# Kernel tuning notes

Measured on AMD Instinct MI355X. Metric: run time of the kernel, lower is better.

The kernel has to match this reference:

```python
import jax, jax.numpy as jnp
import numpy as np

N = 50000
E = 800000
EPS = 1e-12


def sage_conv(x, src, dst, W_l, b_l, W_r):
    # PyG SAGEConv (mean aggr): out = lin_l(mean_{j in N(i)} x_j) + lin_r(x_i)
    msg = x[src]                                             # [E, d] gather
    agg = jax.ops.segment_sum(msg, dst, num_segments=N)      # [N, d]
    cnt = jax.ops.segment_sum(jnp.ones((E,), x.dtype), dst, num_segments=N)
    mean = agg / jnp.maximum(cnt, 1.0)[:, None]              # isolated nodes -> 0
    return mean @ W_l + b_l + x @ W_r


def setup_inputs() -> dict:
    key = jax.random.key(0)
    ks = jax.random.split(key, 12)
    s = 0.05
    return {
        "x": jax.random.normal(ks[0], (N, 128), dtype=jnp.float32),
        "edge_index": jax.random.randint(ks[1], (2, E), 0, N, dtype=jnp.int64),
        # pre: Linear(128 -> 128)
        "pre_W": jax.random.normal(ks[2], (128, 128), dtype=jnp.float32) * s,
        "pre_b": jnp.zeros((128,), dtype=jnp.float32),
        # conv_first: SAGEConv(128 -> 256)
        "W1_l": jax.random.normal(ks[3], (128, 256), dtype=jnp.float32) * s,
        "b1": jnp.zeros((256,), dtype=jnp.float32),
        "W1_r": jax.random.normal(ks[4], (128, 256), dtype=jnp.float32) * s,
        # conv_hidden[0]: SAGEConv(256 -> 256)
        "W2_l": jax.random.normal(ks[5], (256, 256), dtype=jnp.float32) * s,
        "b2": jnp.zeros((256,), dtype=jnp.float32),
        "W2_r": jax.random.normal(ks[6], (256, 256), dtype=jnp.float32) * s,
        # conv_out: SAGEConv(256 -> 256)
        "W3_l": jax.random.normal(ks[7], (256, 256), dtype=jnp.float32) * s,
        "b3": jnp.zeros((256,), dtype=jnp.float32),
        "W3_r": jax.random.normal(ks[8], (256, 256), dtype=jnp.float32) * s,
    }


def reference(x, edge_index, pre_W, pre_b, W1_l, b1, W1_r, W2_l, b2, W2_r, W3_l, b3, W3_r):
    src, dst = edge_index[0], edge_index[1]
    h = x @ pre_W + pre_b                                   # feature_pre Linear
    h = jax.nn.relu(sage_conv(h, src, dst, W1_l, b1, W1_r))  # dropout = identity (eval)
    h = jax.nn.relu(sage_conv(h, src, dst, W2_l, b2, W2_r))
    h = sage_conv(h, src, dst, W3_l, b3, W3_r)
    norm = jnp.sqrt(jnp.sum(h * h, axis=-1, keepdims=True))
    return h / jnp.maximum(norm, EPS)                       # F.normalize(p=2, dim=-1)
```

## Files before the change

kernel.cpp:

```cpp
#include <hip/hip_runtime.h>
#include <cstddef>
#include <cstdint>


typedef __attribute__((ext_vector_type(8))) short short8;
typedef __attribute__((ext_vector_type(4))) float f32x4;

__device__ __forceinline__ unsigned rne_bf16(float f) {
    unsigned b = __float_as_uint(f);
    return (b + 0x7fffu + ((b >> 16) & 1u)) >> 16;
}
__device__ __forceinline__ float bf16_lo(unsigned u) { return __uint_as_float(u << 16); }
__device__ __forceinline__ float bf16_hi(unsigned u) { return __uint_as_float(u & 0xffff0000u); }

__device__ __forceinline__ void stage16(const void* g, unsigned short* ldsbase,
                                        int lane) {
#if __has_builtin(__builtin_amdgcn_global_load_lds)
    (void)lane;
    __builtin_amdgcn_global_load_lds(
        (const __attribute__((address_space(1))) unsigned int*)g,
        (__attribute__((address_space(3))) unsigned int*)ldsbase, 16, 0, 0);
#else
    *(uint4*)(ldsbase + (size_t)lane * 8) = *(const uint4*)g;
#endif
}


__global__ __launch_bounds__(256) void deg_kernel(const int* __restrict__ dst,
                                                  int* __restrict__ deg, int E) {
    int e = blockIdx.x * 256 + threadIdx.x;
    if (e < E) atomicAdd(&deg[dst[e]], 1);
}

__global__ __launch_bounds__(256) void bsum_kernel(const int* __restrict__ deg,
                                                   int* __restrict__ bsum, int n) {
    int i = blockIdx.x * 256 + threadIdx.x;
    int v = (i < n) ? deg[i] : 0;
#pragma unroll
    for (int s = 32; s > 0; s >>= 1) v += __shfl_down(v, s);
    __shared__ int ws[4];
    int lane = threadIdx.x & 63, w = threadIdx.x >> 6;
    if (lane == 0) ws[w] = v;
    __syncthreads();
    if (threadIdx.x == 0) bsum[blockIdx.x] = ws[0] + ws[1] + ws[2] + ws[3];
}

__global__ __launch_bounds__(256) void bscan_kernel(const int* __restrict__ bsum,
                                                    int* __restrict__ boff,
                                                    int* __restrict__ off,
                                                    int nb, int n, int E) {
    int t = threadIdx.x;
    int v = (t < nb) ? bsum[t] : 0;
    int incl = v;
#pragma unroll
    for (int s = 1; s < 64; s <<= 1) {
        int u = __shfl_up(incl, s);
        if ((t & 63) >= s) incl += u;
    }
    __shared__ int ws[4];
    int lane = t & 63, w = t >> 6;
    if (lane == 63) ws[w] = incl;
    __syncthreads();
    int woff = 0;
    for (int j = 0; j < w; ++j) woff += ws[j];
    if (t < nb) boff[t] = woff + incl - v;
    if (t == 0) off[n] = E;
}

__global__ __launch_bounds__(256) void scan_kernel(const int* __restrict__ deg,
                                                   const int* __restrict__ boff,
                                                   int* __restrict__ off,
                                                   float* __restrict__ inv, int n) {
    int i = blockIdx.x * 256 + threadIdx.x;
    int v = (i < n) ? deg[i] : 0;
    int incl = v;
#pragma unroll
    for (int s = 1; s < 64; s <<= 1) {
        int u = __shfl_up(incl, s);
        if ((threadIdx.x & 63) >= s) incl += u;
    }
    __shared__ int ws[4];
    int lane = threadIdx.x & 63, w = threadIdx.x >> 6;
    if (lane == 63) ws[w] = incl;
    __syncthreads();
    int woff = 0;
    for (int j = 0; j < w; ++j) woff += ws[j];
    if (i < n) {
        off[i] = boff[blockIdx.x] + woff + incl - v;
        inv[i] = 1.0f / fmaxf((float)v, 1.0f);
    }
}

__global__ __launch_bounds__(256) void fill_kernel(const int* __restrict__ src,
                                                   const int* __restrict__ dst,
                                                   const int* __restrict__ off,
                                                   int* __restrict__ deg,
                                                   int* __restrict__ ssrc, int E) {
    int e = blockIdx.x * 256 + threadIdx.x;
    if (e >= E) return;
    int d = dst[e];
    int pos = off[d] + atomicSub(&deg[d], 1) - 1;
    ssrc[pos] = src[e];
}


__global__ __launch_bounds__(256) void prep_all(
    const float* __restrict__ x, uint2* __restrict__ xb, int n4, int XB,
    const float* __restrict__ pre_W, const float* __restrict__ W1_l,
    const float* __restrict__ W1_r, const float* __restrict__ W2_l,
    const float* __restrict__ W2_r, const float* __restrict__ W3_l,
    const float* __restrict__ W3_r,
    unsigned short* __restrict__ WT0, unsigned short* __restrict__ WT1,
    unsigned short* __restrict__ WT2, unsigned short* __restrict__ WT3,
    unsigned short* __restrict__ WT4, unsigned short* __restrict__ WT5,
    unsigned short* __restrict__ WT6) {
    if (blockIdx.x < (unsigned)XB) {
        int i = blockIdx.x * 256 + threadIdx.x;
        if (i >= n4) return;
        float4 v = ((const float4*)x)[i];
        uint2 o;
        o.x = rne_bf16(v.x) | (rne_bf16(v.y) << 16);
        o.y = rne_bf16(v.z) | (rne_bf16(v.w) << 16);
        xb[i] = o;
        return;
    }
    int idx = (blockIdx.x - XB) * 256 + threadIdx.x;
    if (idx < 16384) {
        int k = idx >> 7, n = idx & 127;
        WT0[n * 128 + k] = (unsigned short)rne_bf16(pre_W[idx]);
        return;
    }
    idx -= 16384;
    if (idx < 32768) {
        int k = idx >> 8, n = idx & 255;
        WT1[n * 128 + k] = (unsigned short)rne_bf16(W1_l[idx]);
        return;
    }
    idx -= 32768;
    if (idx < 32768) {
        int k = idx >> 8, n = idx & 255;
        WT2[n * 128 + k] = (unsigned short)rne_bf16(W1_r[idx]);
        return;
    }
    idx -= 32768;
    if (idx < 65536) {
        int k = idx >> 8, n = idx & 255;
        WT3[n * 256 + k] = (unsigned short)rne_bf16(W2_l[idx]);
        return;
    }
    idx -= 65536;
    if (idx < 65536) {
        int k = idx >> 8, n = idx & 255;
        WT4[n * 256 + k] = (unsigned short)rne_bf16(W2_r[idx]);
        return;
    }
    idx -= 65536;
    if (idx < 65536) {
        int k = idx >> 8, n = idx & 255;
        WT5[n * 256 + k] = (unsigned short)rne_bf16(W3_l[idx]);
        return;
    }
    idx -= 65536;
    if (idx < 65536) {
        int k = idx >> 8, n = idx & 255;
        WT6[n * 256 + k] = (unsigned short)rne_bf16(W3_r[idx]);
    }
}


template <int D>
__global__ __launch_bounds__(256) void gather_b(const unsigned short* __restrict__ h,
                                                const int* __restrict__ off,
                                                const int* __restrict__ ssrc,
                                                const float* __restrict__ inv,
                                                unsigned short* __restrict__ agg, int n) {
    int node = blockIdx.x * 4 + (threadIdx.x >> 6);
    if (node >= n) return;
    int lane = threadIdx.x & 63;
    int beg = off[node], end = off[node + 1];
    float sc = inv[node];

    if (D == 256) {
        const int half = lane >> 5;
        const int sub  = lane & 31;
        const unsigned short* col = h + (sub << 3);
        float a[8] = {0, 0, 0, 0, 0, 0, 0, 0};
        float b[8] = {0, 0, 0, 0, 0, 0, 0, 0};
        int k = beg;
        for (; k + 3 < end; k += 4) {
            int s0 = ssrc[k + half];
            int s1 = ssrc[k + 2 + half];
            uint4 u = *(const uint4*)(col + (size_t)s0 * 256);
            uint4 v = *(const uint4*)(col + (size_t)s1 * 256);
            a[0] += bf16_lo(u.x); a[1] += bf16_hi(u.x);
            a[2] += bf16_lo(u.y); a[3] += bf16_hi(u.y);
            a[4] += bf16_lo(u.z); a[5] += bf16_hi(u.z);
            a[6] += bf16_lo(u.w); a[7] += bf16_hi(u.w);
            b[0] += bf16_lo(v.x); b[1] += bf16_hi(v.x);
            b[2] += bf16_lo(v.y); b[3] += bf16_hi(v.y);
            b[4] += bf16_lo(v.z); b[5] += bf16_hi(v.z);
            b[6] += bf16_lo(v.w); b[7] += bf16_hi(v.w);
        }
        for (; k < end; k += 2) {
            int e = k + half;
            if (e < end) {
                uint4 u = *(const uint4*)(col + (size_t)ssrc[e] * 256);
                a[0] += bf16_lo(u.x); a[1] += bf16_hi(u.x);
                a[2] += bf16_lo(u.y); a[3] += bf16_hi(u.y);
                a[4] += bf16_lo(u.z); a[5] += bf16_hi(u.z);
                a[6] += bf16_lo(u.w); a[7] += bf16_hi(u.w);
            }
        }
#pragma unroll
        for (int i = 0; i < 8; ++i) a[i] += b[i];
#pragma unroll
        for (int i = 0; i < 8; ++i) a[i] += __shfl_xor(a[i], 32);
        if (half == 0) {
#pragma unroll
            for (int i = 0; i < 8; ++i) a[i] *= sc;
            uint4 o;
            o.x = rne_bf16(a[0]) | (rne_bf16(a[1]) << 16);
            o.y = rne_bf16(a[2]) | (rne_bf16(a[3]) << 16);
            o.z = rne_bf16(a[4]) | (rne_bf16(a[5]) << 16);
            o.w = rne_bf16(a[6]) | (rne_bf16(a[7]) << 16);
            *(uint4*)(agg + (size_t)node * 256 + (sub << 3)) = o;
        }
    } else {
        const int q   = lane >> 4;
        const int sub = lane & 15;
        const unsigned short* col = h + (sub << 3);
        float a[8] = {0, 0, 0, 0, 0, 0, 0, 0};
        float b[8] = {0, 0, 0, 0, 0, 0, 0, 0};
        int k = beg;
        for (; k + 7 < end; k += 8) {
            int s0 = ssrc[k + q];
            int s1 = ssrc[k + 4 + q];
            uint4 u = *(const uint4*)(col + (size_t)s0 * 128);
            uint4 v = *(const uint4*)(col + (size_t)s1 * 128);
            a[0] += bf16_lo(u.x); a[1] += bf16_hi(u.x);
            a[2] += bf16_lo(u.y); a[3] += bf16_hi(u.y);
            a[4] += bf16_lo(u.z); a[5] += bf16_hi(u.z);
            a[6] += bf16_lo(u.w); a[7] += bf16_hi(u.w);
            b[0] += bf16_lo(v.x); b[1] += bf16_hi(v.x);
            b[2] += bf16_lo(v.y); b[3] += bf16_hi(v.y);
            b[4] += bf16_lo(v.z); b[5] += bf16_hi(v.z);
            b[6] += bf16_lo(v.w); b[7] += bf16_hi(v.w);
        }
        for (; k < end; k += 4) {
            int e = k + q;
            if (e < end) {
                uint4 u = *(const uint4*)(col + (size_t)ssrc[e] * 128);
                a[0] += bf16_lo(u.x); a[1] += bf16_hi(u.x);
                a[2] += bf16_lo(u.y); a[3] += bf16_hi(u.y);
                a[4] += bf16_lo(u.z); a[5] += bf16_hi(u.z);
                a[6] += bf16_lo(u.w); a[7] += bf16_hi(u.w);
            }
        }
#pragma unroll
        for (int i = 0; i < 8; ++i) a[i] += b[i];
#pragma unroll
        for (int i = 0; i < 8; ++i) a[i] += __shfl_xor(a[i], 16);
#pragma unroll
        for (int i = 0; i < 8; ++i) a[i] += __shfl_xor(a[i], 32);
        if (q == 0) {
#pragma unroll
            for (int i = 0; i < 8; ++i) a[i] *= sc;
            uint4 o;
            o.x = rne_bf16(a[0]) | (rne_bf16(a[1]) << 16);
            o.y = rne_bf16(a[2]) | (rne_bf16(a[3]) << 16);
            o.z = rne_bf16(a[4]) | (rne_bf16(a[5]) << 16);
            o.w = rne_bf16(a[6]) | (rne_bf16(a[7]) << 16);
            *(uint4*)(agg + (size_t)node * 128 + (sub << 3)) = o;
        }
    }
}

__global__ __launch_bounds__(256) void gemm_bt(
    const unsigned short* __restrict__ A1, const unsigned short* __restrict__ W1T,
    const float* __restrict__ bias, unsigned short* __restrict__ outb,
    int M, int K, int Nn) {
    __shared__ __align__(16) unsigned short As[128 * 64];
    __shared__ __align__(16) unsigned short Bs[128 * 64];

    const int t = threadIdx.x;
    const int lane = t & 63;
    const int w = t >> 6;
    const int wm = w >> 1, wn = w & 1;
    const int m0 = blockIdx.x * 128;
    const int n0 = blockIdx.y * 128;

    f32x4 acc[4][4];
#pragma unroll
    for (int i = 0; i < 4; ++i)
#pragma unroll
        for (int j = 0; j < 4; ++j) acc[i][j] = (f32x4){0.f, 0.f, 0.f, 0.f};

    for (int k0 = 0; k0 < K; k0 += 64) {
#pragma unroll
        for (int r = 0; r < 4; ++r) {
            int p = r * 256 + t;
            int row = p >> 3, slot = p & 7;
            int c = slot ^ (row & 7);
            int gm = m0 + row;
            if (gm >= M) gm = M - 1;
            uint4 va = *(const uint4*)(A1 + (size_t)gm * K + k0 + c * 8);
            uint4 vb = *(const uint4*)(W1T + (size_t)(n0 + row) * K + k0 + c * 8);
            *(uint4*)&As[(size_t)p * 8] = va;
            *(uint4*)&Bs[(size_t)p * 8] = vb;
        }
        __syncthreads();
#pragma unroll
        for (int kk = 0; kk < 2; ++kk) {
            short8 af[4], bfr[4];
            int ac = kk * 4 + (lane >> 4);
#pragma unroll
            for (int i = 0; i < 4; ++i) {
                int arow = wm * 64 + i * 16 + (lane & 15);
                af[i] = *(const short8*)&As[arow * 64 + ((ac ^ (arow & 7)) << 3)];
                int brow = wn * 64 + i * 16 + (lane & 15);
                bfr[i] = *(const short8*)&Bs[brow * 64 + ((ac ^ (brow & 7)) << 3)];
            }
#pragma unroll
            for (int mi = 0; mi < 4; ++mi)
#pragma unroll
                for (int ni = 0; ni < 4; ++ni)
                    acc[mi][ni] = __builtin_amdgcn_mfma_f32_16x16x32_bf16(
                        af[mi], bfr[ni], acc[mi][ni], 0, 0, 0);
        }
        __syncthreads();
    }

#pragma unroll
    for (int ni = 0; ni < 4; ++ni) {
        int n = n0 + wn * 64 + ni * 16 + (lane & 15);
        float bv = (bias != nullptr) ? bias[n] : 0.0f;
#pragma unroll
        for (int mi = 0; mi < 4; ++mi) {
            int mbase = m0 + wm * 64 + mi * 16 + ((lane >> 4) << 2);
#pragma unroll
            for (int r = 0; r < 4; ++r) {
                int m = mbase + r;
                if (m >= M) continue;
                outb[(size_t)m * Nn + n] = (unsigned short)rne_bf16(acc[mi][ni][r] + bv);
            }
        }
    }
}

__global__ __launch_bounds__(512) void gemm_wide(
    const unsigned short* __restrict__ A1, const unsigned short* __restrict__ W1T,
    const unsigned short* __restrict__ A2, const unsigned short* __restrict__ W2T,
    const float* __restrict__ bias,
    unsigned short* __restrict__ outb, float* __restrict__ outf,
    int M, int K, int relu) {
    __shared__ __align__(16) unsigned short As[128 * 64];
    __shared__ __align__(16) unsigned short Bs[256 * 64];
    __shared__ float rs[128][4];

    const int t = threadIdx.x;
    const int lane = t & 63;
    const int w8 = t >> 6;
    const int wm = w8 >> 2, wn = w8 & 3;
    const int m0 = blockIdx.x * 128;

    f32x4 acc[4][4];
#pragma unroll
    for (int i = 0; i < 4; ++i)
#pragma unroll
        for (int j = 0; j < 4; ++j) acc[i][j] = (f32x4){0.f, 0.f, 0.f, 0.f};

    for (int pass = 0; pass < 2; ++pass) {
        const unsigned short* A = pass ? A2 : A1;
        const unsigned short* W = pass ? W2T : W1T;

        for (int k0 = 0; k0 < K; k0 += 64) {
#pragma unroll
            for (int i = 0; i < 2; ++i) {
                int base = (w8 * 2 + i) * 64;
                int p = base + lane;
                int row = p >> 3, slot = p & 7;
                int c = slot ^ (row & 7);
                int gm = m0 + row;
                if (gm >= M) gm = M - 1;
                stage16(A + (size_t)gm * K + k0 + c * 8, &As[(size_t)base * 8], lane);
            }
#pragma unroll
            for (int i = 0; i < 4; ++i) {
                int base = (w8 * 4 + i) * 64;
                int p = base + lane;
                int row = p >> 3, slot = p & 7;
                int c = slot ^ (row & 7);
                stage16(W + (size_t)row * K + k0 + c * 8, &Bs[(size_t)base * 8], lane);
            }
            __syncthreads();
#pragma unroll
            for (int kk = 0; kk < 2; ++kk) {
                short8 af[4], bfr[4];
                int ac = kk * 4 + (lane >> 4);
#pragma unroll
                for (int i = 0; i < 4; ++i) {
                    int arow = wm * 64 + i * 16 + (lane & 15);
                    af[i] = *(const short8*)&As[arow * 64 + ((ac ^ (arow & 7)) << 3)];
                    int brow = wn * 64 + i * 16 + (lane & 15);
                    bfr[i] = *(const short8*)&Bs[brow * 64 + ((ac ^ (brow & 7)) << 3)];
                }
#pragma unroll
                for (int mi = 0; mi < 4; ++mi)
#pragma unroll
                    for (int ni = 0; ni < 4; ++ni)
                        acc[mi][ni] = __builtin_amdgcn_mfma_f32_16x16x32_bf16(
                            af[mi], bfr[ni], acc[mi][ni], 0, 0, 0);
            }
            __syncthreads();
        }
    }

    if (outb) {
#pragma unroll
        for (int ni = 0; ni < 4; ++ni) {
            int n = wn * 64 + ni * 16 + (lane & 15);
            float bv = bias[n];
#pragma unroll
            for (int mi = 0; mi < 4; ++mi) {
                int mbase = m0 + wm * 64 + mi * 16 + ((lane >> 4) << 2);
#pragma unroll
                for (int r = 0; r < 4; ++r) {
                    int m = mbase + r;
                    if (m >= M) continue;
                    float v = acc[mi][ni][r] + bv;
                    if (relu) v = fmaxf(v, 0.0f);
                    outb[(size_t)m * 256 + n] = (unsigned short)rne_bf16(v);
                }
            }
        }
        return;
    }

#pragma unroll
    for (int ni = 0; ni < 4; ++ni) {
        float bv = bias[wn * 64 + ni * 16 + (lane & 15)];
#pragma unroll
        for (int mi = 0; mi < 4; ++mi)
#pragma unroll
            for (int r = 0; r < 4; ++r) acc[mi][ni][r] += bv;
    }
#pragma unroll
    for (int mi = 0; mi < 4; ++mi) {
#pragma unroll
        for (int r = 0; r < 4; ++r) {
            float p = acc[mi][0][r] * acc[mi][0][r] + acc[mi][1][r] * acc[mi][1][r] +
                      acc[mi][2][r] * acc[mi][2][r] + acc[mi][3][r] * acc[mi][3][r];
            p += __shfl_xor(p, 1);
            p += __shfl_xor(p, 2);
            p += __shfl_xor(p, 4);
            p += __shfl_xor(p, 8);
            if ((lane & 15) == 0)
                rs[wm * 64 + mi * 16 + ((lane >> 4) << 2) + r][wn] = p;
        }
    }
    __syncthreads();
#pragma unroll
    for (int mi = 0; mi < 4; ++mi) {
        int mbase = m0 + wm * 64 + mi * 16 + ((lane >> 4) << 2);
        int lrow = wm * 64 + mi * 16 + ((lane >> 4) << 2);
#pragma unroll
        for (int r = 0; r < 4; ++r) {
            int m = mbase + r;
            if (m >= M) continue;
            float s = rs[lrow + r][0] + rs[lrow + r][1] + rs[lrow + r][2] + rs[lrow + r][3];
            float sc = 1.0f / fmaxf(sqrtf(s), 1e-12f);
#pragma unroll
            for (int ni = 0; ni < 4; ++ni) {
                int n = wn * 64 + ni * 16 + (lane & 15);
                outf[(size_t)m * 256 + n] = acc[mi][ni][r] * sc;
            }
        }
    }
}

extern "C" void kernel_launch(void* const* d_in, const int* in_sizes, int n_in,
                              void* d_out, int out_size, void* d_ws, size_t ws_size,
                              hipStream_t stream) {
    const int N = 50000;
    const int E = 800000;
    const int NB = (N + 255) / 256;

    const float* x     = (const float*)d_in[0];
    const int*   ei    = (const int*)d_in[1];
    const float* pre_W = (const float*)d_in[2];
    const float* pre_b = (const float*)d_in[3];
    const float* W1_l  = (const float*)d_in[4];
    const float* b1    = (const float*)d_in[5];
    const float* W1_r  = (const float*)d_in[6];
    const float* W2_l  = (const float*)d_in[7];
    const float* b2    = (const float*)d_in[8];
    const float* W2_r  = (const float*)d_in[9];
    const float* W3_l  = (const float*)d_in[10];
    const float* b3    = (const float*)d_in[11];
    const float* W3_r  = (const float*)d_in[12];
    float* out = (float*)d_out;

    const int* src = ei;
    const int* dst = ei + E;

    int* deg  = (int*)d_ws;
    int* off  = deg + N;
    int* bsum = off + N + 1;
    int* boff = bsum + 256;
    int* ssrc = boff + 256;
    size_t int_words = (size_t)2 * N + 1 + 512 + E;
    int_words = (int_words + 3) & ~(size_t)3;

    float* inv = (float*)d_ws + int_words;
    unsigned short* us = (unsigned short*)(inv + N);

    unsigned short* xb  = us;                 us += (size_t)N * 128;
    unsigned short* WT0 = us;                 us += 16384;
    unsigned short* WT1 = us;                 us += 32768;
    unsigned short* WT2 = us;                 us += 32768;
    unsigned short* WT3 = us;                 us += 65536;
    unsigned short* WT4 = us;                 us += 65536;
    unsigned short* WT5 = us;                 us += 65536;
    unsigned short* WT6 = us;                 us += 65536;
    unsigned short* h0b   = us;               us += (size_t)N * 128;
    unsigned short* agg1b = us;               us += (size_t)N * 128;
    unsigned short* h1b   = us;               us += (size_t)N * 256;
    unsigned short* agg2b = us;               us += (size_t)N * 256;
    unsigned short* h2b   = us;               us += (size_t)N * 256;
    unsigned short* agg3b = us;               us += (size_t)N * 256;

    hipMemsetAsync(deg, 0, (size_t)N * sizeof(int), stream);
    deg_kernel<<<(E + 255) / 256, 256, 0, stream>>>(dst, deg, E);
    bsum_kernel<<<NB, 256, 0, stream>>>(deg, bsum, N);
    bscan_kernel<<<1, 256, 0, stream>>>(bsum, boff, off, NB, N, E);
    scan_kernel<<<NB, 256, 0, stream>>>(deg, boff, off, inv, N);
    fill_kernel<<<(E + 255) / 256, 256, 0, stream>>>(src, dst, off, deg, ssrc, E);

    const int n4 = N * 128 / 4;
    const int XB = (n4 + 255) / 256;
    const int WB = (344064 + 255) / 256;
    prep_all<<<XB + WB, 256, 0, stream>>>(x, (uint2*)xb, n4, XB,
                                          pre_W, W1_l, W1_r, W2_l, W2_r, W3_l,
                                          W3_r, WT0, WT1, WT2, WT3, WT4, WT5, WT6);

    const int MT = (N + 127) / 128;
    const int AG = (N + 3) / 4;

    gemm_bt<<<dim3(MT, 1), 256, 0, stream>>>(xb, WT0, pre_b, h0b, N, 128, 128);

    gather_b<128><<<AG, 256, 0, stream>>>(h0b, off, ssrc, inv, agg1b, N);
    gemm_wide<<<MT, 512, 0, stream>>>(agg1b, WT1, h0b, WT2, b1, h1b, nullptr,
                                      N, 128, 1);

    gather_b<256><<<AG, 256, 0, stream>>>(h1b, off, ssrc, inv, agg2b, N);
    gemm_wide<<<MT, 512, 0, stream>>>(agg2b, WT3, h1b, WT4, b2, h2b, nullptr,
                                      N, 256, 1);

    gather_b<256><<<AG, 256, 0, stream>>>(h2b, off, ssrc, inv, agg3b, N);
    gemm_wide<<<MT, 512, 0, stream>>>(agg3b, WT5, h2b, WT6, b3, nullptr, out,
                                      N, 256, 0);
}
```

Baseline: 497.1 us.

## Co-schedule independent GEMM and gather/CSR work in fused launches

The degree-count kernel is merged into the prep kernel, and the CSR fill kernel into the pre-linear GEMM, as extra block ranges of a single launch. In each SAGE layer the root-weight GEMM (x @ W_r + b) now runs in the same launch as the neighbour gather, with its result written to an fp32 scratch buffer. The follow-up GEMM does only the aggregated-neighbour half and adds that scratch. The aim is to overlap independent memory-bound and compute-bound work and to cut launch count. The cost is an extra fp32 N×256 buffer that is written and read back each layer.

```diff
diff --git a/kernel.cpp b/kernel.cpp
--- a/kernel.cpp
+++ b/kernel.cpp
@@ -26,12 +26,6 @@
 }
 
 
-__global__ __launch_bounds__(256) void deg_kernel(const int* __restrict__ dst,
-                                                  int* __restrict__ deg, int E) {
-    int e = blockIdx.x * 256 + threadIdx.x;
-    if (e < E) atomicAdd(&deg[dst[e]], 1);
-}
-
 __global__ __launch_bounds__(256) void bsum_kernel(const int* __restrict__ deg,
                                                    int* __restrict__ bsum, int n) {
     int i = blockIdx.x * 256 + threadIdx.x;
@@ -91,21 +85,9 @@
     }
 }
 
-__global__ __launch_bounds__(256) void fill_kernel(const int* __restrict__ src,
-                                                   const int* __restrict__ dst,
-                                                   const int* __restrict__ off,
-                                                   int* __restrict__ deg,
-                                                   int* __restrict__ ssrc, int E) {
-    int e = blockIdx.x * 256 + threadIdx.x;
-    if (e >= E) return;
-    int d = dst[e];
-    int pos = off[d] + atomicSub(&deg[d], 1) - 1;
-    ssrc[pos] = src[e];
-}
-
-
-__global__ __launch_bounds__(256) void prep_all(
-    const float* __restrict__ x, uint2* __restrict__ xb, int n4, int XB,
+
+__global__ __launch_bounds__(256) void fatA(
+    const float* __restrict__ x, uint2* __restrict__ xb, int n4, int XB, int PB,
     const float* __restrict__ pre_W, const float* __restrict__ W1_l,
     const float* __restrict__ W1_r, const float* __restrict__ W2_l,
     const float* __restrict__ W2_r, const float* __restrict__ W3_l,
@@ -113,7 +95,13 @@
     unsigned short* __restrict__ WT0, unsigned short* __restrict__ WT1,
     unsigned short* __restrict__ WT2, unsigned short* __restrict__ WT3,
     unsigned short* __restrict__ WT4, unsigned short* __restrict__ WT5,
-    unsigned short* __restrict__ WT6) {
+    unsigned short* __restrict__ WT6,
+    const int* __restrict__ dst, int* __restrict__ deg, int E) {
+    if (blockIdx.x >= (unsigned)PB) {
+        int e = (blockIdx.x - PB) * 256 + threadIdx.x;
+        if (e < E) atomicAdd(&deg[dst[e]], 1);
+        return;
+    }
     if (blockIdx.x < (unsigned)XB) {
         int i = blockIdx.x * 256 + threadIdx.x;
         if (i >= n4) return;
@@ -167,14 +155,114 @@
     }
 }
 
+__device__ __forceinline__ void gemm128_body(
+    unsigned short* As, unsigned short* Bs,
+    const unsigned short* __restrict__ A, const unsigned short* __restrict__ WT,
+    const float* __restrict__ bias, float* __restrict__ Yout,
+    unsigned short* __restrict__ outb, int M, int K, int Nn, int m0, int n0) {
+    const int t = threadIdx.x;
+    const int lane = t & 63;
+    const int w = t >> 6;
+    const int wm = w >> 1, wn = w & 1;
+
+    f32x4 acc[4][4];
+#pragma unroll
+    for (int i = 0; i < 4; ++i)
+#pragma unroll
+        for (int j = 0; j < 4; ++j) acc[i][j] = (f32x4){0.f, 0.f, 0.f, 0.f};
+
+    for (int k0 = 0; k0 < K; k0 += 64) {
+#pragma unroll
+        for (int r = 0; r < 4; ++r) {
+            int p = r * 256 + t;
+            int row = p >> 3, slot = p & 7;
+            int c = slot ^ (row & 7);
+            int gm = m0 + row;
+            if (gm >= M) gm = M - 1;
+            uint4 va = *(const uint4*)(A + (size_t)gm * K + k0 + c * 8);
+            uint4 vb = *(const uint4*)(WT + (size_t)(n0 + row) * K + k0 + c * 8);
+            *(uint4*)&As[(size_t)p * 8] = va;
+            *(uint4*)&Bs[(size_t)p * 8] = vb;
+        }
+        __syncthreads();
+#pragma unroll
+        for (int kk = 0; kk < 2; ++kk) {
+            short8 af[4], bfr[4];
+            int ac = kk * 4 + (lane >> 4);
+#pragma unroll
+            for (int i = 0; i < 4; ++i) {
+                int arow = wm * 64 + i * 16 + (lane & 15);
+                af[i] = *(const short8*)&As[arow * 64 + ((ac ^ (arow & 7)) << 3)];
+                int brow = wn * 64 + i * 16 + (lane & 15);
+                bfr[i] = *(const short8*)&Bs[brow * 64 + ((ac ^ (brow & 7)) << 3)];
+            }
+#pragma unroll
+            for (int mi = 0; mi < 4; ++mi)
+#pragma unroll
+                for (int ni = 0; ni < 4; ++ni)
+                    acc[mi][ni] = __builtin_amdgcn_mfma_f32_16x16x32_bf16(
+                        af[mi], bfr[ni], acc[mi][ni], 0, 0, 0);
+        }
+        __syncthreads();
+    }
+
+#pragma unroll
+    for (int ni = 0; ni < 4; ++ni) {
+        int n = n0 + wn * 64 + ni * 16 + (lane & 15);
+        float bv = bias[n];
+#pragma unroll
+        for (int mi = 0; mi < 4; ++mi) {
+            int mbase = m0 + wm * 64 + mi * 16 + ((lane >> 4) << 2);
+#pragma unroll
+            for (int r = 0; r < 4; ++r) {
+                int m = mbase + r;
+                if (m >= M) continue;
+                float v = acc[mi][ni][r] + bv;
+                if (Yout) Yout[(size_t)m * Nn + n] = v;
+                else      outb[(size_t)m * Nn + n] = (unsigned short)rne_bf16(v);
+            }
+        }
+    }
+}
+
+
+__global__ __launch_bounds__(256) void fatB(
+    const unsigned short* __restrict__ xb, const unsigned short* __restrict__ WT0,
+    const float* __restrict__ pre_b, unsigned short* __restrict__ h0b, int M,
+    int GB,
+    const int* __restrict__ src, const int* __restrict__ dst,
+    const int* __restrict__ off, int* __restrict__ deg,
+    int* __restrict__ ssrc, int E) {
+    __shared__ __align__(16) unsigned short As[128 * 64];
+    __shared__ __align__(16) unsigned short Bs[128 * 64];
+    if (blockIdx.x < (unsigned)GB) {
+        gemm128_body(As, Bs, xb, WT0, pre_b, nullptr, h0b, M, 128, 128,
+                     blockIdx.x * 128, 0);
+        return;
+    }
+    int e = (blockIdx.x - GB) * 256 + threadIdx.x;
+    if (e >= E) return;
+    int d = dst[e];
+    int pos = off[d] + atomicSub(&deg[d], 1) - 1;
+    ssrc[pos] = src[e];
+}
+
 
 template <int D>
-__global__ __launch_bounds__(256) void gather_b(const unsigned short* __restrict__ h,
-                                                const int* __restrict__ off,
-                                                const int* __restrict__ ssrc,
-                                                const float* __restrict__ inv,
-                                                unsigned short* __restrict__ agg, int n) {
-    int node = blockIdx.x * 4 + (threadIdx.x >> 6);
+__global__ __launch_bounds__(256) void fat_gy(
+    const unsigned short* __restrict__ h, const unsigned short* __restrict__ WrT,
+    const float* __restrict__ bias, float* __restrict__ Yf, int M, int K, int GB,
+    const int* __restrict__ off, const int* __restrict__ ssrc,
+    const float* __restrict__ inv, unsigned short* __restrict__ agg, int n) {
+    __shared__ __align__(16) unsigned short As[128 * 64];
+    __shared__ __align__(16) unsigned short Bs[128 * 64];
+    if (blockIdx.x < (unsigned)GB) {
+        int p = blockIdx.x;
+        gemm128_body(As, Bs, h, WrT, bias, Yf, nullptr, M, K, 256,
+                     (p >> 1) * 128, (p & 1) * 128);
+        return;
+    }
+    int node = (blockIdx.x - GB) * 4 + (threadIdx.x >> 6);
     if (node >= n) return;
     int lane = threadIdx.x & 63;
     int beg = off[node], end = off[node + 1];
@@ -275,19 +363,20 @@
     }
 }
 
-__global__ __launch_bounds__(256) void gemm_bt(
-    const unsigned short* __restrict__ A1, const unsigned short* __restrict__ W1T,
-    const float* __restrict__ bias, unsigned short* __restrict__ outb,
-    int M, int K, int Nn) {
+__global__ __launch_bounds__(512) void gemm_lw(
+    const unsigned short* __restrict__ A, const unsigned short* __restrict__ WlT,
+    const float* __restrict__ Yf,
+    unsigned short* __restrict__ outb, float* __restrict__ outf,
+    int M, int K, int relu) {
     __shared__ __align__(16) unsigned short As[128 * 64];
-    __shared__ __align__(16) unsigned short Bs[128 * 64];
+    __shared__ __align__(16) unsigned short Bs[256 * 64];
+    __shared__ float rs[128][4];
 
     const int t = threadIdx.x;
     const int lane = t & 63;
-    const int w = t >> 6;
-    const int wm = w >> 1, wn = w & 1;
+    const int w8 = t >> 6;
+    const int wm = w8 >> 2, wn = w8 & 3;
     const int m0 = blockIdx.x * 128;
-    const int n0 = blockIdx.y * 128;
 
     f32x4 acc[4][4];
 #pragma unroll
@@ -297,16 +386,22 @@
 
     for (int k0 = 0; k0 < K; k0 += 64) {
 #pragma unroll
-        for (int r = 0; r < 4; ++r) {
-            int p = r * 256 + t;
+        for (int i = 0; i < 2; ++i) {
+            int base = (w8 * 2 + i) * 64;
+            int p = base + lane;
             int row = p >> 3, slot = p & 7;
             int c = slot ^ (row & 7);
             int gm = m0 + row;
             if (gm >= M) gm = M - 1;
-            uint4 va = *(const uint4*)(A1 + (size_t)gm * K + k0 + c * 8);
-            uint4 vb = *(const uint4*)(W1T + (size_t)(n0 + row) * K + k0 + c * 8);
-            *(uint4*)&As[(size_t)p * 8] = va;
-            *(uint4*)&Bs[(size_t)p * 8] = vb;
+            stage16(A + (size_t)gm * K + k0 + c * 8, &As[(size_t)base * 8], lane);
+        }
+#pragma unroll
+        for (int i = 0; i < 4; ++i) {
+            int base = (w8 * 4 + i) * 64;
+            int p = base + lane;
+            int row = p >> 3, slot = p & 7;
+            int c = slot ^ (row & 7);
+            stage16(WlT + (size_t)row * K + k0 + c * 8, &Bs[(size_t)base * 8], lane);
         }
         __syncthreads();
 #pragma unroll
@@ -332,86 +427,15 @@
 
 #pragma unroll
     for (int ni = 0; ni < 4; ++ni) {
-        int n = n0 + wn * 64 + ni * 16 + (lane & 15);
-        float bv = (bias != nullptr) ? bias[n] : 0.0f;
+        int n = wn * 64 + ni * 16 + (lane & 15);
 #pragma unroll
         for (int mi = 0; mi < 4; ++mi) {
             int mbase = m0 + wm * 64 + mi * 16 + ((lane >> 4) << 2);
 #pragma unroll
             for (int r = 0; r < 4; ++r) {
                 int m = mbase + r;
-                if (m >= M) continue;
-                outb[(size_t)m * Nn + n] = (unsigned short)rne_bf16(acc[mi][ni][r] + bv);
-            }
-        }
-    }
-}
-
-__global__ __launch_bounds__(512) void gemm_wide(
-    const unsigned short* __restrict__ A1, const unsigned short* __restrict__ W1T,
-    const unsigned short* __restrict__ A2, const unsigned short* __restrict__ W2T,
-    const float* __restrict__ bias,
-    unsigned short* __restrict__ outb, float* __restrict__ outf,
-    int M, int K, int relu) {
-    __shared__ __align__(16) unsigned short As[128 * 64];
-    __shared__ __align__(16) unsigned short Bs[256 * 64];
-    __shared__ float rs[128][4];
-
-    const int t = threadIdx.x;
-    const int lane = t & 63;
-    const int w8 = t >> 6;
-    const int wm = w8 >> 2, wn = w8 & 3;
-    const int m0 = blockIdx.x * 128;
-
-    f32x4 acc[4][4];
-#pragma unroll
-    for (int i = 0; i < 4; ++i)
-#pragma unroll
-        for (int j = 0; j < 4; ++j) acc[i][j] = (f32x4){0.f, 0.f, 0.f, 0.f};
-
-    for (int pass = 0; pass < 2; ++pass) {
-        const unsigned short* A = pass ? A2 : A1;
-        const unsigned short* W = pass ? W2T : W1T;
-
-        for (int k0 = 0; k0 < K; k0 += 64) {
-#pragma unroll
-            for (int i = 0; i < 2; ++i) {
-                int base = (w8 * 2 + i) * 64;
-                int p = base + lane;
-                int row = p >> 3, slot = p & 7;
-                int c = slot ^ (row & 7);
-                int gm = m0 + row;
-                if (gm >= M) gm = M - 1;
-                stage16(A + (size_t)gm * K + k0 + c * 8, &As[(size_t)base * 8], lane);
-            }
-#pragma unroll
-            for (int i = 0; i < 4; ++i) {
-                int base = (w8 * 4 + i) * 64;
-                int p = base + lane;
-                int row = p >> 3, slot = p & 7;
-                int c = slot ^ (row & 7);
-                stage16(W + (size_t)row * K + k0 + c * 8, &Bs[(size_t)base * 8], lane);
-            }
-            __syncthreads();
-#pragma unroll
-            for (int kk = 0; kk < 2; ++kk) {
-                short8 af[4], bfr[4];
-                int ac = kk * 4 + (lane >> 4);
-#pragma unroll
-                for (int i = 0; i < 4; ++i) {
-                    int arow = wm * 64 + i * 16 + (lane & 15);
-                    af[i] = *(const short8*)&As[arow * 64 + ((ac ^ (arow & 7)) << 3)];
-                    int brow = wn * 64 + i * 16 + (lane & 15);
-                    bfr[i] = *(const short8*)&Bs[brow * 64 + ((ac ^ (brow & 7)) << 3)];
-                }
-#pragma unroll
-                for (int mi = 0; mi < 4; ++mi)
-#pragma unroll
-                    for (int ni = 0; ni < 4; ++ni)
-                        acc[mi][ni] = __builtin_amdgcn_mfma_f32_16x16x32_bf16(
-                            af[mi], bfr[ni], acc[mi][ni], 0, 0, 0);
-            }
-            __syncthreads();
+                if (m < M) acc[mi][ni][r] += Yf[(size_t)m * 256 + n];
+            }
         }
     }
 
@@ -419,7 +443,6 @@
 #pragma unroll
         for (int ni = 0; ni < 4; ++ni) {
             int n = wn * 64 + ni * 16 + (lane & 15);
-            float bv = bias[n];
 #pragma unroll
             for (int mi = 0; mi < 4; ++mi) {
                 int mbase = m0 + wm * 64 + mi * 16 + ((lane >> 4) << 2);
@@ -427,7 +450,7 @@
                 for (int r = 0; r < 4; ++r) {
                     int m = mbase + r;
                     if (m >= M) continue;
-                    float v = acc[mi][ni][r] + bv;
+                    float v = acc[mi][ni][r];
                     if (relu) v = fmaxf(v, 0.0f);
                     outb[(size_t)m * 256 + n] = (unsigned short)rne_bf16(v);
                 }
@@ -436,14 +459,6 @@
         return;
     }
 
-#pragma unroll
-    for (int ni = 0; ni < 4; ++ni) {
-        float bv = bias[wn * 64 + ni * 16 + (lane & 15)];
-#pragma unroll
-        for (int mi = 0; mi < 4; ++mi)
-#pragma unroll
-            for (int r = 0; r < 4; ++r) acc[mi][ni][r] += bv;
-    }
 #pragma unroll
     for (int mi = 0; mi < 4; ++mi) {
 #pragma unroll
@@ -512,7 +527,8 @@
     int_words = (int_words + 3) & ~(size_t)3;
 
     float* inv = (float*)d_ws + int_words;
-    unsigned short* us = (unsigned short*)(inv + N);
+    float* Yf  = inv + N;
+    unsigned short* us = (unsigned short*)(Yf + (size_t)N * 256);
 
     unsigned short* xb  = us;                 us += (size_t)N * 128;
     unsigned short* WT0 = us;                 us += 16384;
@@ -529,34 +545,36 @@
     unsigned short* h2b   = us;               us += (size_t)N * 256;
     unsigned short* agg3b = us;               us += (size_t)N * 256;
 
+    const int MT = (N + 127) / 128;
+    const int AG = (N + 3) / 4;
+    const int GB = MT * 2;
+    const int n4 = N * 128 / 4;
+    const int XB = (n4 + 255) / 256;
+    const int WB = (344064 + 255) / 256;
+    const int PB = XB + WB;
+    const int DB = (E + 255) / 256;
+
     hipMemsetAsync(deg, 0, (size_t)N * sizeof(int), stream);
-    deg_kernel<<<(E + 255) / 256, 256, 0, stream>>>(dst, deg, E);
+    fatA<<<PB + DB, 256, 0, stream>>>(x, (uint2*)xb, n4, XB, PB,
+                                      pre_W, W1_l, W1_r, W2_l, W2_r, W3_l, W3_r,
+                                      WT0, WT1, WT2, WT3, WT4, WT5, WT6,
+                                      dst, deg, E);
     bsum_kernel<<<NB, 256, 0, stream>>>(deg, bsum, N);
     bscan_kernel<<<1, 256, 0, stream>>>(bsum, boff, off, NB, N, E);
     scan_kernel<<<NB, 256, 0, stream>>>(deg, boff, off, inv, N);
-    fill_kernel<<<(E + 255) / 256, 256, 0, stream>>>(src, dst, off, deg, ssrc, E);
-
-    const int n4 = N * 128 / 4;
-    const int XB = (n4 + 255) / 256;
-    const int WB = (344064 + 255) / 256;
-    prep_all<<<XB + WB, 256, 0, stream>>>(x, (uint2*)xb, n4, XB,
-                                          pre_W, W1_l, W1_r, W2_l, W2_r, W3_l,
-                                          W3_r, WT0, WT1, WT2, WT3, WT4, WT5, WT6);
-
-    const int MT = (N + 127) / 128;
-    const int AG = (N + 3) / 4;
-
-    gemm_bt<<<dim3(MT, 1), 256, 0, stream>>>(xb, WT0, pre_b, h0b, N, 128, 128);
-
-    gather_b<128><<<AG, 256, 0, stream>>>(h0b, off, ssrc, inv, agg1b, N);
-    gemm_wide<<<MT, 512, 0, stream>>>(agg1b, WT1, h0b, WT2, b1, h1b, nullptr,
-                                      N, 128, 1);
-
-    gather_b<256><<<AG, 256, 0, stream>>>(h1b, off, ssrc, inv, agg2b, N);
-    gemm_wide<<<MT, 512, 0, stream>>>(agg2b, WT3, h1b, WT4, b2, h2b, nullptr,
-                                      N, 256, 1);
-
-    gather_b<256><<<AG, 256, 0, stream>>>(h2b, off, ssrc, inv, agg3b, N);
-    gemm_wide<<<MT, 512, 0, stream>>>(agg3b, WT5, h2b, WT6, b3, nullptr, out,
-                                      N, 256, 0);
-}
+
+    fatB<<<MT + DB, 256, 0, stream>>>(xb, WT0, pre_b, h0b, N, MT,
+                                      src, dst, off, deg, ssrc, E);
+
+    fat_gy<128><<<GB + AG, 256, 0, stream>>>(h0b, WT2, b1, Yf, N, 128, GB,
+                                             off, ssrc, inv, agg1b, N);
+    gemm_lw<<<MT, 512, 0, stream>>>(agg1b, WT1, Yf, h1b, nullptr, N, 128, 1);
+
+    fat_gy<256><<<GB + AG, 256, 0, stream>>>(h1b, WT4, b2, Yf, N, 256, GB,
+                                             off, ssrc, inv, agg2b, N);
+    gemm_lw<<<MT, 512, 0, stream>>>(agg2b, WT3, Yf, h2b, nullptr, N, 256, 1);
+
+    fat_gy<256><<<GB + AG, 256, 0, stream>>>(h2b, WT6, b3, Yf, N, 256, GB,
+                                             off, ssrc, inv, agg3b, N);
+    gemm_lw<<<MT, 512, 0, stream>>>(agg3b, WT5, Yf, nullptr, out, N, 256, 0);
+}
```

Measured after the change: 633.4 us. 1.27x slower.

## Co-schedule root-weight GEMM with neighbor gather in one fused launch

Applied to the files above, without the earlier changes.

Each SAGE layer's x@W_r + bias term is now computed by extra blocks inside the gather kernel, so the independent MFMA work runs alongside the memory-bound neighbor aggregation. The result is written to an fp32 scratch buffer. The following GEMM does only the aggregated-mean @ W_l pass and adds that buffer in its epilogue. This halves the K-loop work of the post-gather GEMM and overlaps it with the gather. In exchange it adds an fp32 N×256 write and read per layer, and the new GEMM blocks load straight from global memory without LDS tiling.

```diff
diff --git a/kernel.cpp b/kernel.cpp
--- a/kernel.cpp
+++ b/kernel.cpp
@@ -167,16 +167,145 @@
     }
 }
 
+__global__ __launch_bounds__(256) void gemm_bt(
+    const unsigned short* __restrict__ A1, const unsigned short* __restrict__ W1T,
+    const float* __restrict__ bias, unsigned short* __restrict__ outb,
+    int M, int K, int Nn) {
+    __shared__ __align__(16) unsigned short As[128 * 64];
+    __shared__ __align__(16) unsigned short Bs[128 * 64];
+
+    const int t = threadIdx.x;
+    const int lane = t & 63;
+    const int w = t >> 6;
+    const int wm = w >> 1, wn = w & 1;
+    const int m0 = blockIdx.x * 128;
+    const int n0 = blockIdx.y * 128;
+
+    f32x4 acc[4][4];
+#pragma unroll
+    for (int i = 0; i < 4; ++i)
+#pragma unroll
+        for (int j = 0; j < 4; ++j) acc[i][j] = (f32x4){0.f, 0.f, 0.f, 0.f};
+
+    for (int k0 = 0; k0 < K; k0 += 64) {
+#pragma unroll
+        for (int r = 0; r < 4; ++r) {
+            int p = r * 256 + t;
+            int row = p >> 3, slot = p & 7;
+            int c = slot ^ (row & 7);
+            int gm = m0 + row;
+            if (gm >= M) gm = M - 1;
+            uint4 va = *(const uint4*)(A1 + (size_t)gm * K + k0 + c * 8);
+            uint4 vb = *(const uint4*)(W1T + (size_t)(n0 + row) * K + k0 + c * 8);
+            *(uint4*)&As[(size_t)p * 8] = va;
+            *(uint4*)&Bs[(size_t)p * 8] = vb;
+        }
+        __syncthreads();
+#pragma unroll
+        for (int kk = 0; kk < 2; ++kk) {
+            short8 af[4], bfr[4];
+            int ac = kk * 4 + (lane >> 4);
+#pragma unroll
+            for (int i = 0; i < 4; ++i) {
+                int arow = wm * 64 + i * 16 + (lane & 15);
+                af[i] = *(const short8*)&As[arow * 64 + ((ac ^ (arow & 7)) << 3)];
+                int brow = wn * 64 + i * 16 + (lane & 15);
+                bfr[i] = *(const short8*)&Bs[brow * 64 + ((ac ^ (brow & 7)) << 3)];
+            }
+#pragma unroll
+            for (int mi = 0; mi < 4; ++mi)
+#pragma unroll
+                for (int ni = 0; ni < 4; ++ni)
+                    acc[mi][ni] = __builtin_amdgcn_mfma_f32_16x16x32_bf16(
+                        af[mi], bfr[ni], acc[mi][ni], 0, 0, 0);
+        }
+        __syncthreads();
+    }
+
+#pragma unroll
+    for (int ni = 0; ni < 4; ++ni) {
+        int n = n0 + wn * 64 + ni * 16 + (lane & 15);
+        float bv = (bias != nullptr) ? bias[n] : 0.0f;
+#pragma unroll
+        for (int mi = 0; mi < 4; ++mi) {
+            int mbase = m0 + wm * 64 + mi * 16 + ((lane >> 4) << 2);
+#pragma unroll
+            for (int r = 0; r < 4; ++r) {
+                int m = mbase + r;
+                if (m >= M) continue;
+                outb[(size_t)m * Nn + n] = (unsigned short)rne_bf16(acc[mi][ni][r] + bv);
+            }
+        }
+    }
+}
+
 
 template <int D>
-__global__ __launch_bounds__(256) void gather_b(const unsigned short* __restrict__ h,
-                                                const int* __restrict__ off,
-                                                const int* __restrict__ ssrc,
-                                                const float* __restrict__ inv,
-                                                unsigned short* __restrict__ agg, int n) {
-    int node = blockIdx.x * 4 + (threadIdx.x >> 6);
+__global__ __launch_bounds__(256) void fat_gy(
+    const unsigned short* __restrict__ h, const unsigned short* __restrict__ WrT,
+    const float* __restrict__ bias, float* __restrict__ Yf, int M, int YB,
+    const int* __restrict__ off, const int* __restrict__ ssrc,
+    const float* __restrict__ inv, unsigned short* __restrict__ agg, int n) {
+    const int lane = threadIdx.x & 63;
+    if ((int)blockIdx.x < YB) {
+        const int p = blockIdx.x;
+        const int m0 = (p >> 1) * 64;
+        const int n0 = (p & 1) * 128;
+        const int w = threadIdx.x >> 6;
+        const int wm = w >> 1, wn = w & 1;
+        const int r16 = lane & 15, kq = lane >> 4;
+
+        f32x4 acc[2][4];
+#pragma unroll
+        for (int i = 0; i < 2; ++i)
+#pragma unroll
+            for (int j = 0; j < 4; ++j) acc[i][j] = (f32x4){0.f, 0.f, 0.f, 0.f};
+
+        int gm0 = m0 + wm * 32 + r16;
+        int gm1 = gm0 + 16;
+        if (gm0 >= M) gm0 = M - 1;
+        if (gm1 >= M) gm1 = M - 1;
+        const unsigned short* a0 = h + (size_t)gm0 * D + kq * 8;
+        const unsigned short* a1 = h + (size_t)gm1 * D + kq * 8;
+        const unsigned short* b0 = WrT + (size_t)(n0 + wn * 64 + r16) * D + kq * 8;
+
+#pragma unroll
+        for (int kk = 0; kk < D / 32; ++kk) {
+            short8 af0 = *(const short8*)(a0 + kk * 32);
+            short8 af1 = *(const short8*)(a1 + kk * 32);
+            short8 bf0 = *(const short8*)(b0 + kk * 32);
+            short8 bf1 = *(const short8*)(b0 + (size_t)16 * D + kk * 32);
+            short8 bf2 = *(const short8*)(b0 + (size_t)32 * D + kk * 32);
+            short8 bf3 = *(const short8*)(b0 + (size_t)48 * D + kk * 32);
+            acc[0][0] = __builtin_amdgcn_mfma_f32_16x16x32_bf16(af0, bf0, acc[0][0], 0, 0, 0);
+            acc[0][1] = __builtin_amdgcn_mfma_f32_16x16x32_bf16(af0, bf1, acc[0][1], 0, 0, 0);
+            acc[0][2] = __builtin_amdgcn_mfma_f32_16x16x32_bf16(af0, bf2, acc[0][2], 0, 0, 0);
+            acc[0][3] = __builtin_amdgcn_mfma_f32_16x16x32_bf16(af0, bf3, acc[0][3], 0, 0, 0);
+            acc[1][0] = __builtin_amdgcn_mfma_f32_16x16x32_bf16(af1, bf0, acc[1][0], 0, 0, 0);
+            acc[1][1] = __builtin_amdgcn_mfma_f32_16x16x32_bf16(af1, bf1, acc[1][1], 0, 0, 0);
+            acc[1][2] = __builtin_amdgcn_mfma_f32_16x16x32_bf16(af1, bf2, acc[1][2], 0, 0, 0);
+            acc[1][3] = __builtin_amdgcn_mfma_f32_16x16x32_bf16(af1, bf3, acc[1][3], 0, 0, 0);
+        }
+
+#pragma unroll
+        for (int j = 0; j < 4; ++j) {
+            int nn = n0 + wn * 64 + j * 16 + (lane & 15);
+            float bv = bias[nn];
+#pragma unroll
+            for (int i = 0; i < 2; ++i) {
+                int mbase = m0 + wm * 32 + i * 16 + ((lane >> 4) << 2);
+#pragma unroll
+                for (int r = 0; r < 4; ++r) {
+                    int m = mbase + r;
+                    if (m < M) Yf[(size_t)m * 256 + nn] = acc[i][j][r] + bv;
+                }
+            }
+        }
+        return;
+    }
+
+    int node = (blockIdx.x - YB) * 4 + (threadIdx.x >> 6);
     if (node >= n) return;
-    int lane = threadIdx.x & 63;
     int beg = off[node], end = off[node + 1];
     float sc = inv[node];
 
@@ -275,19 +404,20 @@
     }
 }
 
-__global__ __launch_bounds__(256) void gemm_bt(
-    const unsigned short* __restrict__ A1, const unsigned short* __restrict__ W1T,
-    const float* __restrict__ bias, unsigned short* __restrict__ outb,
-    int M, int K, int Nn) {
+__global__ __launch_bounds__(512) void gemm_lw(
+    const unsigned short* __restrict__ A, const unsigned short* __restrict__ WlT,
+    const float* __restrict__ Yf,
+    unsigned short* __restrict__ outb, float* __restrict__ outf,
+    int M, int K, int relu) {
     __shared__ __align__(16) unsigned short As[128 * 64];
-    __shared__ __align__(16) unsigned short Bs[128 * 64];
+    __shared__ __align__(16) unsigned short Bs[256 * 64];
+    __shared__ float rs[128][4];
 
     const int t = threadIdx.x;
     const int lane = t & 63;
-    const int w = t >> 6;
-    const int wm = w >> 1, wn = w & 1;
+    const int w8 = t >> 6;
+    const int wm = w8 >> 2, wn = w8 & 3;
     const int m0 = blockIdx.x * 128;
-    const int n0 = blockIdx.y * 128;
 
     f32x4 acc[4][4];
 #pragma unroll
@@ -297,16 +427,22 @@
 
     for (int k0 = 0; k0 < K; k0 += 64) {
 #pragma unroll
-        for (int r = 0; r < 4; ++r) {
-            int p = r * 256 + t;
+        for (int i = 0; i < 2; ++i) {
+            int base = (w8 * 2 + i) * 64;
+            int p = base + lane;
             int row = p >> 3, slot = p & 7;
             int c = slot ^ (row & 7);
             int gm = m0 + row;
             if (gm >= M) gm = M - 1;
-            uint4 va = *(const uint4*)(A1 + (size_t)gm * K + k0 + c * 8);
-            uint4 vb = *(const uint4*)(W1T + (size_t)(n0 + row) * K + k0 + c * 8);
-            *(uint4*)&As[(size_t)p * 8] = va;
-            *(uint4*)&Bs[(size_t)p * 8] = vb;
+            stage16(A + (size_t)gm * K + k0 + c * 8, &As[(size_t)base * 8], lane);
+        }
+#pragma unroll
+        for (int i = 0; i < 4; ++i) {
+            int base = (w8 * 4 + i) * 64;
+            int p = base + lane;
+            int row = p >> 3, slot = p & 7;
+            int c = slot ^ (row & 7);
+            stage16(WlT + (size_t)row * K + k0 + c * 8, &Bs[(size_t)base * 8], lane);
         }
         __syncthreads();
 #pragma unroll
@@ -332,86 +468,15 @@
 
 #pragma unroll
     for (int ni = 0; ni < 4; ++ni) {
-        int n = n0 + wn * 64 + ni * 16 + (lane & 15);
-        float bv = (bias != nullptr) ? bias[n] : 0.0f;
+        int n = wn * 64 + ni * 16 + (lane & 15);
 #pragma unroll
         for (int mi = 0; mi < 4; ++mi) {
             int mbase = m0 + wm * 64 + mi * 16 + ((lane >> 4) << 2);
 #pragma unroll
             for (int r = 0; r < 4; ++r) {
                 int m = mbase + r;
-                if (m >= M) continue;
-                outb[(size_t)m * Nn + n] = (unsigned short)rne_bf16(acc[mi][ni][r] + bv);
-            }
-        }
-    }
-}
-
-__global__ __launch_bounds__(512) void gemm_wide(
-    const unsigned short* __restrict__ A1, const unsigned short* __restrict__ W1T,
-    const unsigned short* __restrict__ A2, const unsigned short* __restrict__ W2T,
-    const float* __restrict__ bias,
-    unsigned short* __restrict__ outb, float* __restrict__ outf,
-    int M, int K, int relu) {
-    __shared__ __align__(16) unsigned short As[128 * 64];
-    __shared__ __align__(16) unsigned short Bs[256 * 64];
-    __shared__ float rs[128][4];
-
-    const int t = threadIdx.x;
-    const int lane = t & 63;
-    const int w8 = t >> 6;
-    const int wm = w8 >> 2, wn = w8 & 3;
-    const int m0 = blockIdx.x * 128;
-
-    f32x4 acc[4][4];
-#pragma unroll
-    for (int i = 0; i < 4; ++i)
-#pragma unroll
-        for (int j = 0; j < 4; ++j) acc[i][j] = (f32x4){0.f, 0.f, 0.f, 0.f};
-
-    for (int pass = 0; pass < 2; ++pass) {
-        const unsigned short* A = pass ? A2 : A1;
-        const unsigned short* W = pass ? W2T : W1T;
-
-        for (int k0 = 0; k0 < K; k0 += 64) {
-#pragma unroll
-            for (int i = 0; i < 2; ++i) {
-                int base = (w8 * 2 + i) * 64;
-                int p = base + lane;
-                int row = p >> 3, slot = p & 7;
-                int c = slot ^ (row & 7);
-                int gm = m0 + row;
-                if (gm >= M) gm = M - 1;
-                stage16(A + (size_t)gm * K + k0 + c * 8, &As[(size_t)base * 8], lane);
-            }
-#pragma unroll
-            for (int i = 0; i < 4; ++i) {
-                int base = (w8 * 4 + i) * 64;
-                int p = base + lane;
-                int row = p >> 3, slot = p & 7;
-                int c = slot ^ (row & 7);
-                stage16(W + (size_t)row * K + k0 + c * 8, &Bs[(size_t)base * 8], lane);
-            }
-            __syncthreads();
-#pragma unroll
-            for (int kk = 0; kk < 2; ++kk) {
-                short8 af[4], bfr[4];
-                int ac = kk * 4 + (lane >> 4);
-#pragma unroll
-                for (int i = 0; i < 4; ++i) {
-                    int arow = wm * 64 + i * 16 + (lane & 15);
-                    af[i] = *(const short8*)&As[arow * 64 + ((ac ^ (arow & 7)) << 3)];
-                    int brow = wn * 64 + i * 16 + (lane & 15);
-                    bfr[i] = *(const short8*)&Bs[brow * 64 + ((ac ^ (brow & 7)) << 3)];
-                }
-#pragma unroll
-                for (int mi = 0; mi < 4; ++mi)
-#pragma unroll
-                    for (int ni = 0; ni < 4; ++ni)
-                        acc[mi][ni] = __builtin_amdgcn_mfma_f32_16x16x32_bf16(
-                            af[mi], bfr[ni], acc[mi][ni], 0, 0, 0);
-            }
-            __syncthreads();
+                if (m < M) acc[mi][ni][r] += Yf[(size_t)m * 256 + n];
+            }
         }
     }
 
@@ -419,7 +484,6 @@
 #pragma unroll
         for (int ni = 0; ni < 4; ++ni) {
             int n = wn * 64 + ni * 16 + (lane & 15);
-            float bv = bias[n];
 #pragma unroll
             for (int mi = 0; mi < 4; ++mi) {
                 int mbase = m0 + wm * 64 + mi * 16 + ((lane >> 4) << 2);
@@ -427,7 +491,7 @@
                 for (int r = 0; r < 4; ++r) {
                     int m = mbase + r;
                     if (m >= M) continue;
-                    float v = acc[mi][ni][r] + bv;
+                    float v = acc[mi][ni][r];
                     if (relu) v = fmaxf(v, 0.0f);
                     outb[(size_t)m * 256 + n] = (unsigned short)rne_bf16(v);
                 }
@@ -436,14 +500,6 @@
         return;
     }
 
-#pragma unroll
-    for (int ni = 0; ni < 4; ++ni) {
-        float bv = bias[wn * 64 + ni * 16 + (lane & 15)];
-#pragma unroll
-        for (int mi = 0; mi < 4; ++mi)
-#pragma unroll
-            for (int r = 0; r < 4; ++r) acc[mi][ni][r] += bv;
-    }
 #pragma unroll
     for (int mi = 0; mi < 4; ++mi) {
 #pragma unroll
@@ -512,7 +568,8 @@
     int_words = (int_words + 3) & ~(size_t)3;
 
     float* inv = (float*)d_ws + int_words;
-    unsigned short* us = (unsigned short*)(inv + N);
+    float* Yf  = inv + N;
+    unsigned short* us = (unsigned short*)(Yf + (size_t)N * 256);
 
     unsigned short* xb  = us;                 us += (size_t)N * 128;
     unsigned short* WT0 = us;                 us += 16384;
@@ -545,18 +602,19 @@
 
     const int MT = (N + 127) / 128;
     const int AG = (N + 3) / 4;
+    const int YB = ((N + 63) / 64) * 2;
 
     gemm_bt<<<dim3(MT, 1), 256, 0, stream>>>(xb, WT0, pre_b, h0b, N, 128, 128);
 
-    gather_b<128><<<AG, 256, 0, stream>>>(h0b, off, ssrc, inv, agg1b, N);
-    gemm_wide<<<MT, 512, 0, stream>>>(agg1b, WT1, h0b, WT2, b1, h1b, nullptr,
-                                      N, 128, 1);
-
-    gather_b<256><<<AG, 256, 0, stream>>>(h1b, off, ssrc, inv, agg2b, N);
-    gemm_wide<<<MT, 512, 0, stream>>>(agg2b, WT3, h1b, WT4, b2, h2b, nullptr,
-                                      N, 256, 1);
-
-    gather_b<256><<<AG, 256, 0, stream>>>(h2b, off, ssrc, inv, agg3b, N);
-    gemm_wide<<<MT, 512, 0, stream>>>(agg3b, WT5, h2b, WT6, b3, nullptr, out,
-                                      N, 256, 0);
-}
+    fat_gy<128><<<YB + AG, 256, 0, stream>>>(h0b, WT2, b1, Yf, N, YB,
+                                             off, ssrc, inv, agg1b, N);
+    gemm_lw<<<MT, 512, 0, stream>>>(agg1b, WT1, Yf, h1b, nullptr, N, 128, 1);
+
+    fat_gy<256><<<YB + AG, 256, 0, stream>>>(h1b, WT4, b2, Yf, N, YB,
+                                             off, ssrc, inv, agg2b, N);
+    gemm_lw<<<MT, 512, 0, stream>>>(agg2b, WT3, Yf, h2b, nullptr, N, 256, 1);
+
+    fat_gy<256><<<YB + AG, 256, 0, stream>>>(h2b, WT6, b3, Yf, N, YB,
+                                             off, ssrc, inv, agg3b, N);
+    gemm_lw<<<MT, 512, 0, stream>>>(agg3b, WT5, Yf, nullptr, out, N, 256, 0);
+}
```

Measured after the change: 638.0 us. 1.28x slower.
